# Performance work log

Hardware: AMD Instinct MI355X
Metric: run time of the kernel (lower is better)

## Reference

```python
import jax, jax.numpy as jnp
import numpy as np

N = 8192          # total proposals
D_IN = 256 * 7 * 7  # 12544
HID = 1024
C = 3


def setup_inputs() -> dict:
    key = jax.random.key(0)
    ks = jax.random.split(key, 9)
    s_in = 1.0 / np.sqrt(D_IN)
    s_h = 1.0 / np.sqrt(HID)
    return {
        "feature_vectors": jax.random.normal(ks[0], (N, D_IN), dtype=jnp.float32),
        "W1": jax.random.uniform(ks[1], (D_IN, HID), jnp.float32, -s_in, s_in),
        "b1": jax.random.uniform(ks[2], (HID,), jnp.float32, -s_in, s_in),
        "W2": jax.random.uniform(ks[3], (HID, HID), jnp.float32, -s_h, s_h),
        "b2": jax.random.uniform(ks[4], (HID,), jnp.float32, -s_h, s_h),
        "Wc": jax.random.uniform(ks[5], (HID, C + 1), jnp.float32, -s_h, s_h),
        "bc": jax.random.uniform(ks[6], (C + 1,), jnp.float32, -s_h, s_h),
        "Wr": jax.random.uniform(ks[7], (HID, 4 * C), jnp.float32, -s_h, s_h),
        "br": jax.random.uniform(ks[8], (4 * C,), jnp.float32, -s_h, s_h),
    }


def reference(feature_vectors, W1, b1, W2, b2, Wc, bc, Wr, br):
    # intermediate: Linear -> Linear -> ReLU (note: no ReLU between the two Linears,
    # matching the original nn.Sequential ordering)
    h = feature_vectors @ W1 + b1          # [N, 1024]
    h = h @ W2 + b2                        # [N, 1024]
    h = jax.nn.relu(h)
    class_logits = jax.nn.softmax(h @ Wc + bc, axis=-1)  # [N, C+1]
    box_pred = h @ Wr + br                  # [N, 4C]
    return class_logits, box_pred
```

## Files before the change

### kernel.cpp

```cpp
#include <hip/hip_runtime.h>
#include <hip/hip_bf16.h>
#include <stdint.h>

using u16 = unsigned short;
using u32 = unsigned int;

typedef __attribute__((ext_vector_type(8))) short short8;
typedef __attribute__((ext_vector_type(4))) float floatx4;

__device__ __forceinline__ u16 f2bf(float f) {
  __hip_bfloat16 h = __float2bfloat16(f);
  return *reinterpret_cast<u16*>(&h);
}

__device__ __forceinline__ void gl_lds16(const void* g, void* l) {
  __builtin_amdgcn_global_load_lds((const __attribute__((address_space(1))) void*)g,
                                   (__attribute__((address_space(3))) void*)l, 16, 0, 0);
}

__global__ __launch_bounds__(256)
void transpose_to_bf16(const float* __restrict__ in, u16* __restrict__ out,
                       int R, int Cc) {
  __shared__ float tile[32][33];
  int c0 = blockIdx.x * 32;
  int r0 = blockIdx.y * 32;
  int tx = threadIdx.x;
  int ty = threadIdx.y;
#pragma unroll
  for (int i = 0; i < 32; i += 8)
    tile[ty + i][tx] = in[(size_t)(r0 + ty + i) * Cc + c0 + tx];
  __syncthreads();
#pragma unroll
  for (int i = 0; i < 32; i += 8)
    out[(size_t)(c0 + ty + i) * R + r0 + tx] = f2bf(tile[tx][ty + i]);
}

__global__ __launch_bounds__(256)
void cvt_bf16(const float4* __restrict__ in, uint2* __restrict__ out, int n4) {
  int i = blockIdx.x * 256 + threadIdx.x;
  if (i >= n4) return;
  float4 v = in[i];
  u32 lo = (u32)f2bf(v.x) | ((u32)f2bf(v.y) << 16);
  u32 hi = (u32)f2bf(v.z) | ((u32)f2bf(v.w) << 16);
  out[i] = make_uint2(lo, hi);
}

constexpr int BM = 128, BN = 128, BK = 32;

template <bool A_BF16, bool RELU>
__global__ __launch_bounds__(256, 3)
void gemm_bt(const void* __restrict__ Aip, const u16* __restrict__ BT,
             const float* __restrict__ bias, u16* __restrict__ C,
             int M, int N, int K) {
  __shared__ __align__(16) u16 As[BM * BK];
  __shared__ __align__(16) u16 Bs[BN * BK];
  const int tid  = threadIdx.x;
  const int lane = tid & 63;
  const int wave = tid >> 6;
  const int m0 = blockIdx.y * BM;
  const int n0 = blockIdx.x * BN;
  const int wm = (wave & 1) * 64;
  const int wn = (wave >> 1) * 64;
  const int row = lane & 15;
  const int kq  = lane >> 4;

  floatx4 acc[4][4] = {};

  int a_off[4], b_off[4];
#pragma unroll
  for (int t = 0; t < 4; ++t) {
    int mr = wm + t * 16 + row;
    a_off[t] = mr * BK + ((kq ^ ((mr >> 1) & 3)) * 8);
    int nr = wn + t * 16 + row;
    b_off[t] = nr * BK + ((kq ^ ((nr >> 1) & 3)) * 8);
  }

  const u16* bptr[2];
  int b_lds[2];
#pragma unroll
  for (int it = 0; it < 2; ++it) {
    int c = it * 256 + tid;
    int nrow = c >> 2;
    int kc = ((c & 3) ^ ((nrow >> 1) & 3)) * 8;
    bptr[it] = BT + (size_t)(n0 + nrow) * K + kc;
    b_lds[it] = (it * 256 + wave * 64) * 8;
  }

  const u16* aptrB[2];
  int a_ldsB[2];
  const float* aptrF[4];
  int a_stF[4];
  if constexpr (A_BF16) {
    const u16* A = (const u16*)Aip;
#pragma unroll
    for (int it = 0; it < 2; ++it) {
      int c = it * 256 + tid;
      int mrow = c >> 2;
      int kc = ((c & 3) ^ ((mrow >> 1) & 3)) * 8;
      aptrB[it] = A + (size_t)(m0 + mrow) * K + kc;
      a_ldsB[it] = (it * 256 + wave * 64) * 8;
    }
  } else {
    const float* A = (const float*)Aip;
#pragma unroll
    for (int it = 0; it < 4; ++it) {
      int idx = it * 256 + tid;
      int mrow = idx >> 3;
      int kc = (idx & 7) * 4;
      aptrF[it] = A + (size_t)(m0 + mrow) * K + kc;
      int chunk = kc >> 3, half = (kc >> 2) & 1;
      int sc = chunk ^ ((mrow >> 1) & 3);
      a_stF[it] = mrow * BK + sc * 8 + half * 4;
    }
  }

  for (int k0 = 0; k0 < K; k0 += BK) {
    __syncthreads();
    if constexpr (A_BF16) {
#pragma unroll
      for (int it = 0; it < 2; ++it)
        gl_lds16(aptrB[it] + k0, &As[a_ldsB[it]]);
    } else {
#pragma unroll
      for (int it = 0; it < 4; ++it) {
        float4 v = *(const float4*)(aptrF[it] + k0);
        u32 lo = (u32)f2bf(v.x) | ((u32)f2bf(v.y) << 16);
        u32 hi = (u32)f2bf(v.z) | ((u32)f2bf(v.w) << 16);
        *(uint2*)&As[a_stF[it]] = make_uint2(lo, hi);
      }
    }
#pragma unroll
    for (int it = 0; it < 2; ++it)
      gl_lds16(bptr[it] + k0, &Bs[b_lds[it]]);
    __syncthreads();

    short8 a[4], b[4];
#pragma unroll
    for (int t = 0; t < 4; ++t) {
      a[t] = *(const short8*)&As[a_off[t]];
      b[t] = *(const short8*)&Bs[b_off[t]];
    }
#pragma unroll
    for (int mt = 0; mt < 4; ++mt)
#pragma unroll
      for (int nt = 0; nt < 4; ++nt)
        acc[mt][nt] = __builtin_amdgcn_mfma_f32_16x16x32_bf16(
            a[mt], b[nt], acc[mt][nt], 0, 0, 0);
  }

  const int ccol = row;
  const int crow = kq * 4;
#pragma unroll
  for (int mt = 0; mt < 4; ++mt) {
#pragma unroll
    for (int nt = 0; nt < 4; ++nt) {
      int gm = m0 + wm + mt * 16 + crow;
      int gn = n0 + wn + nt * 16 + ccol;
      float bv = bias[gn];
#pragma unroll
      for (int r = 0; r < 4; ++r) {
        float v = acc[mt][nt][r] + bv;
        if (RELU) v = fmaxf(v, 0.f);
        C[(size_t)(gm + r) * N + gn] = f2bf(v);
      }
    }
  }
}

__device__ __forceinline__ float wave_sum(float v) {
#pragma unroll
  for (int m = 32; m >= 1; m >>= 1) v += __shfl_xor(v, m, 64);
  return v;
}

__global__ __launch_bounds__(64)
void head_kernel(const u16* __restrict__ H, const float* __restrict__ Wc,
                 const float* __restrict__ bc, const float* __restrict__ Wr,
                 const float* __restrict__ br, float* __restrict__ out) {
  const int rowi = blockIdx.x;
  const int lane = threadIdx.x;
  const u16* h = H + (size_t)rowi * 1024 + lane * 16;
  uint4 p0 = *(const uint4*)h;
  uint4 p1 = *(const uint4*)(h + 8);
  u32 w[8] = {p0.x, p0.y, p0.z, p0.w, p1.x, p1.y, p1.z, p1.w};
  float x[16];
#pragma unroll
  for (int i = 0; i < 8; ++i) {
    union { u32 u; float f; } lo, hi;
    lo.u = w[i] << 16;
    hi.u = w[i] & 0xffff0000u;
    x[2 * i] = lo.f;
    x[2 * i + 1] = hi.f;
  }
  float ac[4] = {};
  float ar[12] = {};
  const int kbase = lane * 16;
#pragma unroll
  for (int j = 0; j < 16; ++j) {
    float xv = x[j];
    const float* wc = Wc + (size_t)(kbase + j) * 4;
#pragma unroll
    for (int c = 0; c < 4; ++c) ac[c] = fmaf(xv, wc[c], ac[c]);
    const float* wr = Wr + (size_t)(kbase + j) * 12;
#pragma unroll
    for (int r = 0; r < 12; ++r) ar[r] = fmaf(xv, wr[r], ar[r]);
  }
#pragma unroll
  for (int c = 0; c < 4; ++c) ac[c] = wave_sum(ac[c]);
#pragma unroll
  for (int r = 0; r < 12; ++r) ar[r] = wave_sum(ar[r]);

  if (lane == 0) {
    float lg[4], mx = -1e30f;
#pragma unroll
    for (int c = 0; c < 4; ++c) { lg[c] = ac[c] + bc[c]; mx = fmaxf(mx, lg[c]); }
    float s = 0.f;
#pragma unroll
    for (int c = 0; c < 4; ++c) { lg[c] = __expf(lg[c] - mx); s += lg[c]; }
    float inv = 1.f / s;
#pragma unroll
    for (int c = 0; c < 4; ++c) out[(size_t)rowi * 4 + c] = lg[c] * inv;
    float* ob = out + 8192 * 4;
#pragma unroll
    for (int r = 0; r < 12; ++r) ob[(size_t)rowi * 12 + r] = ar[r] + br[r];
  }
}

extern "C" void kernel_launch(void* const* d_in, const int* in_sizes, int n_in,
                              void* d_out, int out_size, void* d_ws, size_t ws_size,
                              hipStream_t stream) {
  const float* X  = (const float*)d_in[0];
  const float* W1 = (const float*)d_in[1];
  const float* b1 = (const float*)d_in[2];
  const float* W2 = (const float*)d_in[3];
  const float* b2 = (const float*)d_in[4];
  const float* Wc = (const float*)d_in[5];
  const float* bc = (const float*)d_in[6];
  const float* Wr = (const float*)d_in[7];
  const float* br = (const float*)d_in[8];

  constexpr int NP = 8192, DIN = 12544, HID = 1024;
  char* ws = (char*)d_ws;
  u16* W1T = (u16*)ws;
  u16* W2T = (u16*)(ws + (size_t)HID * DIN * 2);
  u16* H1  = (u16*)((char*)W2T + (size_t)HID * HID * 2);
  u16* Hb  = H1 + (size_t)NP * HID;
  u16* Xb  = Hb + (size_t)NP * HID;
  size_t need_base = (size_t)HID * DIN * 2 + (size_t)HID * HID * 2 +
                     2 * (size_t)NP * HID * 2;
  bool use_xbf = ws_size >= need_base + (size_t)NP * DIN * 2;

  transpose_to_bf16<<<dim3(HID / 32, DIN / 32), dim3(32, 8), 0, stream>>>(W1, W1T, DIN, HID);
  transpose_to_bf16<<<dim3(HID / 32, HID / 32), dim3(32, 8), 0, stream>>>(W2, W2T, HID, HID);

  if (use_xbf) {
    int n4 = NP * DIN / 4;
    cvt_bf16<<<(n4 + 255) / 256, 256, 0, stream>>>((const float4*)X, (uint2*)Xb, n4);
    gemm_bt<true, false><<<dim3(HID / BN, NP / BM), 256, 0, stream>>>(
        Xb, W1T, b1, H1, NP, HID, DIN);
  } else {
    gemm_bt<false, false><<<dim3(HID / BN, NP / BM), 256, 0, stream>>>(
        X, W1T, b1, H1, NP, HID, DIN);
  }
  gemm_bt<true, true><<<dim3(HID / BN, NP / BM), 256, 0, stream>>>(
      H1, W2T, b2, Hb, NP, HID, HID);
  head_kernel<<<NP, 64, 0, stream>>>(Hb, Wc, bc, Wr, br, (float*)d_out);
}
```

Measured before the change: 1.013 ms.

## Add triple-buffered 256x128 GEMM kernel with interleaved MFMA and async staging

Adds a new GEMM kernel for both hidden-layer matmuls. It uses 256x128 tiles with BK=64, 8 waves and triple-buffered LDS filled through global_load_lds. Each k-step is split into four phases that interleave LDS fragment reads, prefetch of the next-next tile and MFMA bursts under raised wave priority, with an XOR swizzle and a remapped block order for cache locality. The aim is to hide global-memory latency and raise MFMA utilisation compared with the single-buffered 128x128 kernel, at the cost of many barriers, larger LDS use (144KB) and hand-tuned waitcnt counts that must stay correct.

```diff
diff --git a/kernel.cpp b/kernel.cpp
--- a/kernel.cpp
+++ b/kernel.cpp
@@ -167,6 +167,171 @@
   }
 }
 
+constexpr int A_BUF  = 256 * 64;
+constexpr int B_BUF  = 128 * 64;
+constexpr int B_BASE = 3 * A_BUF;
+constexpr int LDS_BYTES = (3 * A_BUF + 3 * B_BUF) * 2;
+
+#define MM(i, j, va, vb) \
+  acc[i][j] = __builtin_amdgcn_mfma_f32_16x16x32_bf16(va, vb, acc[i][j], 0, 0, 0)
+#define MEMF() asm volatile("" ::: "memory")
+#define BAR() do { MEMF(); __builtin_amdgcn_s_barrier(); MEMF(); } while (0)
+#define STAGE_AH(h, bufo) \
+  do { gl_lds16(apt[h][0], lds + (bufo) + adst[h][0]); apt[h][0] += 64; \
+       gl_lds16(apt[h][1], lds + (bufo) + adst[h][1]); apt[h][1] += 64; } while (0)
+#define STAGE_BH(h, bufo) \
+  do { gl_lds16(bpt[h], lds + (bufo) + bdst[h]); bpt[h] += 64; } while (0)
+
+template <bool RELU>
+__global__ __launch_bounds__(512, 2)
+void gemm256(const u16* __restrict__ A, const u16* __restrict__ BT,
+             const float* __restrict__ bias, u16* __restrict__ C,
+             int N, int K) {
+  extern __shared__ u16 lds[];
+  const int tid  = threadIdx.x;
+  const int lane = tid & 63;
+  const int wave = tid >> 6;
+  const int wm = wave >> 1;
+  const int wn = wave & 1;
+  const int row = lane & 15;
+  const int kq  = lane >> 4;
+  const int sw  = lane & 7;
+
+  const int orig = blockIdx.y * 8 + blockIdx.x;
+  const int rr = ((orig & 7) << 5) | (orig >> 3);
+  const int n0 = (rr & 7) * 128;
+  const int m0 = (rr >> 3) * 256;
+
+  const int o0 = ((kq) ^ sw) * 8;
+  const int o1 = ((4 | kq) ^ sw) * 8;
+  const int ar0 = (wm * 64 + row) * 64;
+  const int ar1 = ar0 + 16 * 64;
+  const int ar2 = ar0 + 32 * 64;
+  const int ar3 = ar0 + 48 * 64;
+  const int br0 = (wn * 64 + row) * 64;
+  const int br1 = br0 + 16 * 64;
+  const int br2 = br0 + 32 * 64;
+  const int br3 = br0 + 48 * 64;
+
+  const u16* apt[2][2];
+  int adst[2][2];
+#pragma unroll
+  for (int h = 0; h < 2; ++h)
+#pragma unroll
+    for (int L = 0; L < 2; ++L) {
+      int i = L * 512 + tid;
+      int rg = h * 128 + (i >> 3);
+      int c = i & 7;
+      apt[h][L] = A + (size_t)(m0 + rg) * K + ((c ^ (rg & 7)) * 8);
+      adst[h][L] = h * 8192 + L * 4096 + wave * 512;
+    }
+  const u16* bpt[2];
+  int bdst[2];
+#pragma unroll
+  for (int h = 0; h < 2; ++h) {
+    int rg = h * 64 + (tid >> 3);
+    int c = tid & 7;
+    bpt[h] = BT + (size_t)(n0 + rg) * K + ((c ^ (rg & 7)) * 8);
+    bdst[h] = B_BASE + h * 4096 + wave * 512;
+  }
+
+  STAGE_AH(0, 0);      STAGE_AH(1, 0);      STAGE_BH(0, 0);     STAGE_BH(1, 0);
+  STAGE_AH(0, A_BUF);  STAGE_AH(1, A_BUF);  STAGE_BH(0, B_BUF); STAGE_BH(1, B_BUF);
+  asm volatile("s_waitcnt vmcnt(6)" ::: "memory");
+  BAR();
+
+  floatx4 acc[4][4] = {};
+  int cb = 0, sb = 2;
+  const int NT = K >> 6;
+  for (int T = 0; T < NT; ++T) {
+    const bool st = (T + 2 < NT);
+    const u16* Ac = lds + cb * A_BUF;
+    const u16* Bc = lds + B_BASE + cb * B_BUF;
+    const int sA = sb * A_BUF;
+    const int sB = sb * B_BUF;
+
+    short8 a0k0, a0k1, a1k0, a1k1, a2k0, a2k1, a3k0, a3k1;
+    short8 b0k0, b0k1, b1k0, b1k1, b2k0, b2k1, b3k0, b3k1;
+
+    a0k0 = *(const short8*)(Ac + ar0 + o0);
+    a0k1 = *(const short8*)(Ac + ar0 + o1);
+    a1k0 = *(const short8*)(Ac + ar1 + o0);
+    a1k1 = *(const short8*)(Ac + ar1 + o1);
+    b0k0 = *(const short8*)(Bc + br0 + o0);
+    b0k1 = *(const short8*)(Bc + br0 + o1);
+    b1k0 = *(const short8*)(Bc + br1 + o0);
+    b1k1 = *(const short8*)(Bc + br1 + o1);
+    if (st) STAGE_AH(0, sA);
+    BAR();
+    __builtin_amdgcn_s_setprio(1);
+    MM(0, 0, a0k0, b0k0); MM(0, 1, a0k0, b1k0);
+    MM(1, 0, a1k0, b0k0); MM(1, 1, a1k0, b1k0);
+    MM(0, 0, a0k1, b0k1); MM(0, 1, a0k1, b1k1);
+    MM(1, 0, a1k1, b0k1); MM(1, 1, a1k1, b1k1);
+    __builtin_amdgcn_s_setprio(0);
+    BAR();
+
+    b2k0 = *(const short8*)(Bc + br2 + o0);
+    b2k1 = *(const short8*)(Bc + br2 + o1);
+    b3k0 = *(const short8*)(Bc + br3 + o0);
+    b3k1 = *(const short8*)(Bc + br3 + o1);
+    if (st) STAGE_AH(1, sA);
+    BAR();
+    __builtin_amdgcn_s_setprio(1);
+    MM(0, 2, a0k0, b2k0); MM(0, 3, a0k0, b3k0);
+    MM(1, 2, a1k0, b2k0); MM(1, 3, a1k0, b3k0);
+    MM(0, 2, a0k1, b2k1); MM(0, 3, a0k1, b3k1);
+    MM(1, 2, a1k1, b2k1); MM(1, 3, a1k1, b3k1);
+    __builtin_amdgcn_s_setprio(0);
+    BAR();
+
+    a2k0 = *(const short8*)(Ac + ar2 + o0);
+    a2k1 = *(const short8*)(Ac + ar2 + o1);
+    a3k0 = *(const short8*)(Ac + ar3 + o0);
+    a3k1 = *(const short8*)(Ac + ar3 + o1);
+    if (st) STAGE_BH(0, sB);
+    BAR();
+    __builtin_amdgcn_s_setprio(1);
+    MM(2, 2, a2k0, b2k0); MM(2, 3, a2k0, b3k0);
+    MM(3, 2, a3k0, b2k0); MM(3, 3, a3k0, b3k0);
+    MM(2, 2, a2k1, b2k1); MM(2, 3, a2k1, b3k1);
+    MM(3, 2, a3k1, b2k1); MM(3, 3, a3k1, b3k1);
+    __builtin_amdgcn_s_setprio(0);
+    BAR();
+
+    if (st) STAGE_BH(1, sB);
+    BAR();
+    __builtin_amdgcn_s_setprio(1);
+    MM(2, 0, a2k0, b0k0); MM(2, 1, a2k0, b1k0);
+    MM(3, 0, a3k0, b0k0); MM(3, 1, a3k0, b1k0);
+    MM(2, 0, a2k1, b0k1); MM(2, 1, a2k1, b1k1);
+    MM(3, 0, a3k1, b0k1); MM(3, 1, a3k1, b1k1);
+    __builtin_amdgcn_s_setprio(0);
+    if (st) asm volatile("s_waitcnt vmcnt(6)" ::: "memory");
+    else    asm volatile("s_waitcnt vmcnt(0)" ::: "memory");
+    BAR();
+
+    cb = (cb == 2) ? 0 : cb + 1;
+    sb = (sb == 2) ? 0 : sb + 1;
+  }
+
+#pragma unroll
+  for (int mt = 0; mt < 4; ++mt) {
+#pragma unroll
+    for (int nt = 0; nt < 4; ++nt) {
+      int gm = m0 + wm * 64 + mt * 16 + kq * 4;
+      int gn = n0 + wn * 64 + nt * 16 + row;
+      float bv = bias[gn];
+#pragma unroll
+      for (int r = 0; r < 4; ++r) {
+        float v = acc[mt][nt][r] + bv;
+        if (RELU) v = fmaxf(v, 0.f);
+        C[(size_t)(gm + r) * N + gn] = f2bf(v);
+      }
+    }
+  }
+}
+
 __device__ __forceinline__ float wave_sum(float v) {
 #pragma unroll
   for (int m = 32; m >= 1; m >>= 1) v += __shfl_xor(v, m, 64);
@@ -250,19 +415,28 @@
                      2 * (size_t)NP * HID * 2;
   bool use_xbf = ws_size >= need_base + (size_t)NP * DIN * 2;
 
+  static bool s_attr = false;
+  if (!s_attr) {
+    hipFuncSetAttribute(reinterpret_cast<const void*>(gemm256<false>),
+                        hipFuncAttributeMaxDynamicSharedMemorySize, LDS_BYTES);
+    hipFuncSetAttribute(reinterpret_cast<const void*>(gemm256<true>),
+                        hipFuncAttributeMaxDynamicSharedMemorySize, LDS_BYTES);
+    s_attr = true;
+  }
+
   transpose_to_bf16<<<dim3(HID / 32, DIN / 32), dim3(32, 8), 0, stream>>>(W1, W1T, DIN, HID);
   transpose_to_bf16<<<dim3(HID / 32, HID / 32), dim3(32, 8), 0, stream>>>(W2, W2T, HID, HID);
 
   if (use_xbf) {
     int n4 = NP * DIN / 4;
     cvt_bf16<<<(n4 + 255) / 256, 256, 0, stream>>>((const float4*)X, (uint2*)Xb, n4);
-    gemm_bt<true, false><<<dim3(HID / BN, NP / BM), 256, 0, stream>>>(
-        Xb, W1T, b1, H1, NP, HID, DIN);
+    gemm256<false><<<dim3(8, NP / 256), 512, LDS_BYTES, stream>>>(
+        Xb, W1T, b1, H1, HID, DIN);
   } else {
     gemm_bt<false, false><<<dim3(HID / BN, NP / BM), 256, 0, stream>>>(
         X, W1T, b1, H1, NP, HID, DIN);
   }
-  gemm_bt<true, true><<<dim3(HID / BN, NP / BM), 256, 0, stream>>>(
-      H1, W2T, b2, Hb, NP, HID, HID);
+  gemm256<true><<<dim3(8, NP / 256), 512, LDS_BYTES, stream>>>(
+      H1, W2T, b2, Hb, HID, HID);
   head_kernel<<<NP, 64, 0, stream>>>(Hb, Wc, bc, Wr, br, (float*)d_out);
 }
```

Measured after the change: 877.1 us. -13.4%, faster.
